# Optimization experiments

Hardware: AMD Instinct MI355X
Metric: run time of the kernel (lower is better)

## Reference

```python
import jax, jax.numpy as jnp
import numpy as np


def _rope_tables(seq_len, d_k, dtype):
    # Faithful to SimpleRotary intent: only d_k//4 frequencies exist; the
    # remaining d_k//4 of the half-width table is identity (cos=1, sin=0),
    # i.e. zero angular frequency (modded-nanogpt style partial rotary).
    half = d_k // 2
    quarter = d_k // 4
    freqs = (1.0 / 10000.0) ** np.linspace(0.0, 1.0, quarter, dtype=np.float32)
    ang = np.concatenate([freqs, np.zeros(half - quarter, dtype=np.float32)])
    theta = np.arange(seq_len, dtype=np.float32)[:, None] * ang[None, :]  # [S, d_k//2]
    return jnp.asarray(np.cos(theta), dtype), jnp.asarray(np.sin(theta), dtype)


def _apply_rope(x, cos, sin):
    # x: [B, H, S, d_k]; cos/sin: [S, d_k//2]
    x1, x2 = jnp.split(x, 2, axis=-1)
    c = cos[None, None]  # [1,1,S,d_k//2]
    s = sin[None, None]
    return jnp.concatenate([x1 * c - x2 * s, x1 * s + x2 * c], axis=-1)


def setup_inputs() -> dict:
    key = jax.random.key(0)
    k1, k2, k3 = jax.random.split(key, 3)
    B, S, D = 2, 2048, 1024
    x = jax.random.normal(k1, (B, S, D), dtype=jnp.float32)
    Wqkv = jax.random.normal(k2, (3 * D, D), dtype=jnp.float32) * 0.02
    Wo = jax.random.normal(k3, (D, D), dtype=jnp.float32) * 0.02
    return {"x": x, "Wqkv": Wqkv, "Wo": Wo, "n_heads": 16}


def reference(x, Wqkv, Wo, n_heads):
    B, S, D = x.shape
    d_k = D // n_heads
    qkv = jnp.einsum('bsd,ed->bse', x, Wqkv)  # [B,S,3D]
    qkv = qkv.reshape(B, S, 3, n_heads, d_k).transpose(2, 0, 3, 1, 4)  # [3,B,H,S,d_k]
    q, k, v = qkv[0], qkv[1], qkv[2]
    cos, sin = _rope_tables(S, d_k, x.dtype)
    q = _apply_rope(q, cos, sin)
    k = _apply_rope(k, cos, sin)
    scale = 1.0 / float(np.sqrt(d_k))
    scores = jnp.einsum('bhqd,bhkd->bhqk', q, k) * scale  # [B,H,S,S]
    causal = jnp.tril(jnp.ones((S, S), dtype=bool))
    scores = jnp.where(causal[None, None], scores, jnp.finfo(scores.dtype).min)
    probs = jax.nn.softmax(scores, axis=-1)
    out = jnp.einsum('bhqk,bhkd->bhqd', probs, v)  # [B,H,S,d_k]
    out = out.transpose(0, 2, 1, 3).reshape(B, S, D)
    return jnp.einsum('bsd,ed->bse', out, Wo)
```

## Files before the change

### kernel.cpp

```cpp
#include <hip/hip_runtime.h>
#include <hip/hip_bf16.h>


typedef __bf16 bf16x8 __attribute__((ext_vector_type(8)));
typedef float f32x4 __attribute__((ext_vector_type(4)));

#define LOG2E 1.4426950408889634f

__device__ __forceinline__ ushort f2bf(float f) {
  __hip_bfloat16 h = __float2bfloat16(f);
  return __builtin_bit_cast(ushort, h);
}

__device__ __forceinline__ uint pack2(float a, float b) {
  return (uint)f2bf(a) | ((uint)f2bf(b) << 16);
}

__device__ __forceinline__ uint pack2t(float a, float b) {
  return __builtin_amdgcn_perm(__builtin_bit_cast(uint, b),
                               __builtin_bit_cast(uint, a), 0x07060302u);
}

__device__ __forceinline__ float fexp2(float x) {
#if __has_builtin(__builtin_amdgcn_exp2f)
  return __builtin_amdgcn_exp2f(x);
#else
  float r;
  asm volatile("v_exp_f32 %0, %1\n\ts_nop 0" : "=v"(r) : "v"(x));
  return r;
#endif
}

#define CBAR() __asm__ __volatile__("" ::: "memory")

__device__ __forceinline__ void conv_frag_one(const float* __restrict__ src,
                                              ushort* __restrict__ dst, int b,
                                              int t) {
  int r16 = b >> 3, kc = b & 7;
  int c = t >> 6, lane = t & 63, quad = lane >> 4, rr = lane & 15;
  const float* s =
      src + ((long)(r16 * 16 + rr)) * 1024 + kc * 128 + c * 32 + quad * 8;
  float4 a = *(const float4*)s;
  float4 bb = *(const float4*)(s + 4);
  uint4 pk = {pack2(a.x, a.y), pack2(a.z, a.w), pack2(bb.x, bb.y),
              pack2(bb.z, bb.w)};
  *(uint4*)&dst[((long)(r16 * 32 + kc * 4 + c)) * 512 + lane * 8] = pk;
}

__global__ __launch_bounds__(256) void conv_frag3(
    const float* __restrict__ s0, ushort* __restrict__ d0, int nb0,
    const float* __restrict__ s1, ushort* __restrict__ d1, int nb1,
    const float* __restrict__ s2, ushort* __restrict__ d2) {
  int b = blockIdx.x;
  if (b < nb0) {
    conv_frag_one(s0, d0, b, threadIdx.x);
  } else if (b < nb0 + nb1) {
    conv_frag_one(s1, d1, b - nb0, threadIdx.x);
  } else {
    conv_frag_one(s2, d2, b - nb0 - nb1, threadIdx.x);
  }
}

__global__ __launch_bounds__(256) void gemm_bt(
    const ushort* __restrict__ A, const ushort* __restrict__ B,
    ushort* __restrict__ qb, ushort* __restrict__ kb, ushort* __restrict__ vb) {
  __shared__ __align__(16) ushort SMEM[17408];
  const int tid = threadIdx.x;
  const int w = tid >> 6, lane = tid & 63, quad = lane >> 4, lc = lane & 15;
  const int bid = blockIdx.x;
  const int bm = bid / 24, bn = bid % 24;
  const int wm = (w & 1) * 64, wn = (w >> 1) * 64;

  f32x4 acc[4][4] = {};

  const ushort* Ap = A + (long)(bm * 8 + (w & 1) * 4) * 16384 + lane * 8;
  const ushort* Bp = B + (long)(bn * 8 + (w >> 1) * 4) * 16384 + lane * 8;

#define GLD(AF, BF, K32)                                                       \
  {                                                                            \
    for (int t = 0; t < 4; ++t)                                                \
      AF[t] = *(const bf16x8*)&Ap[(long)t * 16384 + (K32) * 512];              \
    for (int t = 0; t < 4; ++t)                                                \
      BF[t] = *(const bf16x8*)&Bp[(long)t * 16384 + (K32) * 512];              \
  }
#define MM(AF, BF)                                                             \
  for (int rt = 0; rt < 4; ++rt)                                               \
    for (int ct = 0; ct < 4; ++ct)                                             \
      acc[rt][ct] = __builtin_amdgcn_mfma_f32_16x16x32_bf16(                   \
          AF[rt], BF[ct], acc[rt][ct], 0, 0, 0);

  bf16x8 a0[4], b0[4], a1[4], b1[4];
  GLD(a0, b0, 0);
  for (int k = 0; k < 32; k += 2) {
    GLD(a1, b1, k + 1);
    MM(a0, b0);
    int kn = (k + 2 < 32) ? k + 2 : 31;
    GLD(a0, b0, kn);
    MM(a1, b1);
  }
#undef GLD
#undef MM

  {
    const int e0 = bn * 128;
    const int g = e0 >> 10;
    const int h0 = (e0 & 1023) >> 6;
    ushort* Ct = SMEM;
    __syncthreads();

    if (g == 2) {
      for (int rt = 0; rt < 4; ++rt)
        for (int ct = 0; ct < 4; ++ct) {
          int col = wn + ct * 16 + lc;
          int r0 = wm + rt * 16 + quad * 4;
          uint2 pk = {pack2(acc[rt][ct][0], acc[rt][ct][1]),
                      pack2(acc[rt][ct][2], acc[rt][ct][3])};
          *(uint2*)&Ct[col * 136 + r0] = pk;
        }
    } else {
      const float qs = (g == 0) ? 0.125f * LOG2E : 1.0f;
      const float ang = powf(1e-4f, (float)lc * (1.0f / 15.0f));
      for (int rt = 0; rt < 4; ++rt)
        for (int r2 = 0; r2 < 4; ++r2) {
          int row = wm + rt * 16 + quad * 4 + r2;
          int srow = (bm * 128 + row) & 2047;
          float theta = (float)srow * ang;
          float sn, c;
          sincosf(theta, &sn, &c);
          float x1 = acc[rt][0][r2], x2 = acc[rt][2][r2];
          acc[rt][0][r2] = x1 * c - x2 * sn;
          acc[rt][2][r2] = x1 * sn + x2 * c;
          for (int ct = 0; ct < 4; ++ct)
            Ct[row * 136 + wn + ct * 16 + lc] = f2bf(acc[rt][ct][r2] * qs);
        }
    }
    __syncthreads();

    if (g == 0) {
      for (int i = 0; i < 8; ++i) {
        int u = i * 256 + tid;
        int row = u >> 4, c8 = u & 15;
        int m = bm * 128 + row;
        int srow = m & 2047, b = m >> 11;
        uint4 vv = *(const uint4*)&Ct[row * 136 + c8 * 8];
        *(uint4*)&qb[(((long)(b * 16 + h0 + (c8 >> 3))) * 2048 + srow) * 64 +
                     (c8 & 7) * 8] = vv;
      }
    } else if (g == 1) {
      for (int i = 0; i < 8; ++i) {
        int u = i * 256 + tid;
        int head = u >> 10, off = u & 1023;
        int jrel = off >> 9, kc = (off >> 8) & 1, t = (off >> 6) & 3;
        int quadK = (off >> 4) & 3, lcA = off & 15;
        int srl = jrel * 64 + t * 16 + lcA;
        uint4 vv = *(const uint4*)&Ct[srl * 136 + head * 64 + kc * 32 + quadK * 8];
        int m = bm * 128 + srl;
        int srow = m & 2047, b = m >> 11;
        int bh = b * 16 + h0 + head;
        int chunk = (srow >> 6) * 8 + kc * 4 + t;
        *(uint4*)&kb[(long)bh * 131072 + chunk * 512 + (quadK * 16 + lcA) * 8] = vv;
      }
    } else {
      for (int i = 0; i < 8; ++i) {
        int u = i * 256 + tid;
        int head = u >> 10, off = u & 1023;
        int jrel = off >> 9, kcV = (off >> 8) & 1, mt = (off >> 6) & 3;
        int quadV = (off >> 4) & 3, lcA = off & 15;
        int srl = jrel * 64 + kcV * 32 + quadV * 8;
        int d = mt * 16 + lcA;
        uint4 vv = *(const uint4*)&Ct[(head * 64 + d) * 136 + srl];
        int m = bm * 128 + srl;
        int srow = m & 2047, b = m >> 11;
        int bh = b * 16 + h0 + head;
        int chunk = (srow >> 6) * 8 + kcV * 4 + mt;
        *(uint4*)&vb[(long)bh * 131072 + chunk * 512 + (quadV * 16 + lcA) * 8] = vv;
      }
    }
  }
}

__global__ __launch_bounds__(64) void gemm_proj(
    const ushort* __restrict__ A, const ushort* __restrict__ B,
    float* __restrict__ Cout) {
  __shared__ __align__(16) float T[64 * 68];
  const int lane = threadIdx.x, quad = lane >> 4, lc = lane & 15;
  const int bid = blockIdx.x;
  const int r = bid >> 3;
  const int bm = (bid & 7) * 8 + (r >> 4);
  const int bn = r & 15;

  f32x4 acc[4][4] = {};

  const ushort* Ap = A + (long)(bm * 4) * 16384 + lane * 8;
  const ushort* Bp = B + (long)(bn * 4) * 16384 + lane * 8;

#define GLD(AF, BF, K32)                                                       \
  {                                                                            \
    for (int t = 0; t < 4; ++t)                                                \
      AF[t] = *(const bf16x8*)&Ap[(long)t * 16384 + (K32) * 512];              \
    for (int t = 0; t < 4; ++t)                                                \
      BF[t] = *(const bf16x8*)&Bp[(long)t * 16384 + (K32) * 512];              \
  }
#define MM(AF, BF)                                                             \
  for (int rt = 0; rt < 4; ++rt)                                               \
    for (int ct = 0; ct < 4; ++ct)                                             \
      acc[rt][ct] = __builtin_amdgcn_mfma_f32_16x16x32_bf16(                   \
          AF[rt], BF[ct], acc[rt][ct], 0, 0, 0);

  bf16x8 a0[4], b0[4], a1[4], b1[4];
  GLD(a0, b0, 0);
  for (int k = 0; k < 32; k += 2) {
    GLD(a1, b1, k + 1);
    MM(a0, b0);
    int kn = (k + 2 < 32) ? k + 2 : 31;
    GLD(a0, b0, kn);
    MM(a1, b1);
  }
#undef GLD
#undef MM

  for (int rt = 0; rt < 4; ++rt)
    for (int ct = 0; ct < 4; ++ct)
      for (int r2 = 0; r2 < 4; ++r2)
        T[(rt * 16 + quad * 4 + r2) * 68 + ct * 16 + lc] = acc[rt][ct][r2];
  CBAR();
  for (int p = 0; p < 16; ++p) {
    int row = p * 4 + quad;
    float4 v = *(const float4*)&T[row * 68 + lc * 4];
    *(float4*)&Cout[(long)(bm * 64 + row) * 1024 + bn * 64 + lc * 4] = v;
  }
}

__global__ __launch_bounds__(64) void attn_kernel(
    const ushort* __restrict__ qb, const ushort* __restrict__ kb,
    const ushort* __restrict__ vt, ushort* __restrict__ out) {
  __shared__ __align__(16) ushort Psw2[2][32 * 64];
  const int lane = threadIdx.x;
  const int quad = lane >> 4, lc = lane & 15, l7 = lc & 7;
  const int bid = blockIdx.x;
  const int s = 63 - (bid >> 5);
  const int bh = bid & 31;
  const int bidx = bh >> 4, h = bh & 15;
  const int qtbase = s * 32;

  bf16x8 qf[2][2];
  for (int kc = 0; kc < 2; ++kc)
    for (int q2 = 0; q2 < 2; ++q2)
      qf[kc][q2] = *(const bf16x8*)&qb[((long)bh * 2048 + qtbase + q2 * 16 + lc) * 64 +
                                       kc * 32 + quad * 8];

  f32x4 oacc[4][2] = {};
  float l_lane[2] = {0.0f, 0.0f};

  const ushort* K = kb + (long)bh * 131072;
  const ushort* Vt = vt + (long)bh * 131072;
  const int jmax = s >> 1;
  const int rowoff = (s & 1) * 32;
  const int lane8 = lane * 8;

#define LOADTILE(KF, VF, JT)                                                   \
  {                                                                            \
    const ushort* Kp_ = K + (JT) * 4096 + lane8;                               \
    const ushort* Vp_ = Vt + (JT) * 4096 + lane8;                              \
    for (int kc = 0; kc < 2; ++kc)                                             \
      for (int t = 0; t < 4; ++t) {                                            \
        KF[kc][t] = *(const bf16x8*)&Kp_[(kc * 4 + t) * 512];                  \
        VF[kc][t] = *(const bf16x8*)&Vp_[(kc * 4 + t) * 512];                  \
      }                                                                        \
  }

#define COMPUTE(KF, VF, J, PAR)                                                \
  {                                                                            \
    f32x4 sacc[4][2] = {};                                                     \
    __builtin_amdgcn_s_setprio(1);                                             \
    for (int kc = 0; kc < 2; ++kc)                                             \
      for (int kt = 0; kt < 4; ++kt)                                           \
        for (int q2 = 0; q2 < 2; ++q2)                                         \
          sacc[kt][q2] = __builtin_amdgcn_mfma_f32_16x16x32_bf16(              \
              KF[kc][kt], qf[kc][q2], sacc[kt][q2], 0, 0, 0);                  \
    __builtin_amdgcn_s_setprio(0);                                             \
    if ((J) == jmax) {                                \
      for (int kt = 0; kt < 4; ++kt)                                           \
        for (int q2 = 0; q2 < 2; ++q2) {                                       \
          int rowrel = rowoff + q2 * 16 + lc;                                  \
          for (int r = 0; r < 4; ++r)                                          \
            if (kt * 16 + quad * 4 + r > rowrel) sacc[kt][q2][r] = -1.0e30f;   \
        }                                                                      \
    }                                                                          \
    ushort* Psw = Psw2[PAR];                                                   \
    for (int q2 = 0; q2 < 2; ++q2) {                                           \
      float p[4][4];                                                           \
      float rs = 0.0f;                                                         \
      for (int kt = 0; kt < 4; ++kt)                                           \
        for (int r = 0; r < 4; ++r) {                                          \
          p[kt][r] = fexp2(sacc[kt][q2][r]);                                   \
          rs += p[kt][r];                                                      \
        }                                                                      \
      l_lane[q2] += rs;                                                        \
      for (int kt = 0; kt < 4; ++kt) {                                         \
        uint2 pk = {pack2t(p[kt][0], p[kt][1]), pack2t(p[kt][2], p[kt][3])};   \
        *(uint2*)&Psw[(q2 * 16 + lc) * 64 +                                    \
                      (((kt * 2 + (quad >> 1)) ^ l7) << 3) +                   \
                      ((quad & 1) << 2)] = pk;                                 \
      }                                                                        \
    }                                                                          \
    CBAR();       \
    __builtin_amdgcn_s_setprio(1);                                             \
    for (int kc = 0; kc < 2; ++kc) {                                           \
      bf16x8 pf[2];                                                            \
      for (int q2 = 0; q2 < 2; ++q2)                                           \
        pf[q2] = *(const bf16x8*)&Psw[(q2 * 16 + lc) * 64 +                    \
                                      (((kc * 4 + quad) ^ l7) << 3)];          \
      for (int mt = 0; mt < 4; ++mt)                                           \
        for (int q2 = 0; q2 < 2; ++q2)                                         \
          oacc[mt][q2] = __builtin_amdgcn_mfma_f32_16x16x32_bf16(              \
              VF[kc][mt], pf[q2], oacc[mt][q2], 0, 0, 0);                      \
    }                                                                          \
    __builtin_amdgcn_s_setprio(0);                                             \
  }

  bf16x8 kA[2][4], vA[2][4], kB[2][4], vB[2][4];
  LOADTILE(kA, vA, 0);
  int j = 0;
  while (true) {
    int jn = (j < jmax) ? j + 1 : j;
    LOADTILE(kB, vB, jn);
    COMPUTE(kA, vA, j, 0);
    if (j >= jmax) break;
    ++j;
    int jn2 = (j < jmax) ? j + 1 : j;
    LOADTILE(kA, vA, jn2);
    COMPUTE(kB, vB, j, 1);
    if (j >= jmax) break;
    ++j;
  }
#undef LOADTILE
#undef COMPUTE

  float l_[2];
  for (int q2 = 0; q2 < 2; ++q2) {
    float rs = l_lane[q2];
    rs += __shfl_xor(rs, 16, 64);
    rs += __shfl_xor(rs, 32, 64);
    l_[q2] = rs;
  }
  ushort* Psw = Psw2[0];
  CBAR();
  for (int q2 = 0; q2 < 2; ++q2) {
    float linv = 1.0f / l_[q2];
    for (int mt = 0; mt < 4; ++mt) {
      uint2 pk = {pack2(oacc[mt][q2][0] * linv, oacc[mt][q2][1] * linv),
                  pack2(oacc[mt][q2][2] * linv, oacc[mt][q2][3] * linv)};
      *(uint2*)&Psw[(q2 * 16 + lc) * 64 + (((mt * 2 + (quad >> 1)) ^ l7) << 3) +
                    ((quad & 1) << 2)] = pk;
    }
  }
  CBAR();
  {
    int r2 = lane >> 1;
    long m = (long)bidx * 2048 + qtbase + r2;
    int m4 = (int)(m >> 4), rr = (int)(m & 15);
    for (int c = 0; c < 4; ++c) {
      int c8 = (lane & 1) * 4 + c;
      uint4 vv = *(const uint4*)&Psw[r2 * 64 + ((c8 ^ (r2 & 7)) << 3)];
      *(uint4*)&out[((long)m4 * 32 + h * 2 + (c8 >> 2)) * 512 +
                    ((c8 & 3) * 16 + rr) * 8] = vv;
    }
  }
}

extern "C" void kernel_launch(void* const* d_in, const int* in_sizes, int n_in,
                              void* d_out, int out_size, void* d_ws, size_t ws_size,
                              hipStream_t stream) {
  const float* x = nullptr;
  const float* Wqkv = nullptr;
  const float* Wo = nullptr;
  for (int i = 0; i < n_in; ++i) {
    if (in_sizes[i] == 4194304) x = (const float*)d_in[i];
    else if (in_sizes[i] == 3145728) Wqkv = (const float*)d_in[i];
    else if (in_sizes[i] == 1048576) Wo = (const float*)d_in[i];
  }
  float* out = (float*)d_out;

  ushort* qbuf = (ushort*)d_ws;
  ushort* kbuf = qbuf + 4194304;
  ushort* vbuf = kbuf + 4194304;
  ushort* scr4 = vbuf + 4194304;
  ushort* wqkvh = scr4;
  ushort* ao   = scr4;
  ushort* xh   = (ushort*)d_out;
  ushort* woh  = xh + 4194304;

  conv_frag3<<<4096, 256, 0, stream>>>(x, xh, 2048, Wqkv, wqkvh, 1536, Wo, woh);
  gemm_bt<<<768, 256, 0, stream>>>(xh, wqkvh, qbuf, kbuf, vbuf);
  attn_kernel<<<2048, 64, 0, stream>>>(qbuf, kbuf, vbuf, ao);
  gemm_proj<<<1024, 64, 0, stream>>>(ao, woh, out);
}
```

Baseline: 189.1 us.

## Split attention KV loop across two waves with LDS reduction

The attention block grows from one wave to two. Each wave handles alternating KV tiles (even and odd) for the same 32 query rows, and the partial outputs and row sums are combined through shared memory before normalisation and the store. This is meant to shorten the serial KV loop per block on long causal rows and add more waves for latency hiding. In exchange it adds a cross-wave reduction, extra LDS, and __syncthreads. The first blocks (s=0,1) leave wave 1 idle. Since there is no max subtraction, the partial sums can be added directly.

```diff
diff --git a/kernel.cpp b/kernel.cpp
--- a/kernel.cpp
+++ b/kernel.cpp
@@ -231,32 +231,36 @@
   }
 }
 
-__global__ __launch_bounds__(64) void attn_kernel(
+__global__ __launch_bounds__(128) void attn_kernel(
     const ushort* __restrict__ qb, const ushort* __restrict__ kb,
     const ushort* __restrict__ vt, ushort* __restrict__ out) {
-  __shared__ __align__(16) ushort Psw2[2][32 * 64];
-  const int lane = threadIdx.x;
+  __shared__ __align__(16) ushort PswAll[2][2][32 * 64];
+  __shared__ float lbuf[128];
+  const int tid = threadIdx.x;
+  const int w = tid >> 6;
+  const int lane = tid & 63;
   const int quad = lane >> 4, lc = lane & 15, l7 = lc & 7;
   const int bid = blockIdx.x;
   const int s = 63 - (bid >> 5);
   const int bh = bid & 31;
   const int bidx = bh >> 4, h = bh & 15;
   const int qtbase = s * 32;
-
-  bf16x8 qf[2][2];
-  for (int kc = 0; kc < 2; ++kc)
-    for (int q2 = 0; q2 < 2; ++q2)
-      qf[kc][q2] = *(const bf16x8*)&qb[((long)bh * 2048 + qtbase + q2 * 16 + lc) * 64 +
-                                       kc * 32 + quad * 8];
-
-  f32x4 oacc[4][2] = {};
-  float l_lane[2] = {0.0f, 0.0f};
-
-  const ushort* K = kb + (long)bh * 131072;
-  const ushort* Vt = vt + (long)bh * 131072;
   const int jmax = s >> 1;
   const int rowoff = (s & 1) * 32;
   const int lane8 = lane * 8;
+
+  f32x4 oacc[4][2] = {};
+  float l_lane[2] = {0.0f, 0.0f};
+
+  const ushort* K = kb + (long)bh * 131072;
+  const ushort* Vt = vt + (long)bh * 131072;
+
+  if (w <= jmax) {
+    bf16x8 qf[2][2];
+    for (int kc = 0; kc < 2; ++kc)
+      for (int q2 = 0; q2 < 2; ++q2)
+        qf[kc][q2] = *(const bf16x8*)&qb[((long)bh * 2048 + qtbase + q2 * 16 + lc) * 64 +
+                                         kc * 32 + quad * 8];
 
 #define LOADTILE(KF, VF, JT)                                                   \
   {                                                                            \
@@ -279,7 +283,7 @@
           sacc[kt][q2] = __builtin_amdgcn_mfma_f32_16x16x32_bf16(              \
               KF[kc][kt], qf[kc][q2], sacc[kt][q2], 0, 0, 0);                  \
     __builtin_amdgcn_s_setprio(0);                                             \
-    if ((J) == jmax) {                                \
+    if ((J) == jmax) {              \
       for (int kt = 0; kt < 4; ++kt)                                           \
         for (int q2 = 0; q2 < 2; ++q2) {                                       \
           int rowrel = rowoff + q2 * 16 + lc;                                  \
@@ -287,7 +291,7 @@
             if (kt * 16 + quad * 4 + r > rowrel) sacc[kt][q2][r] = -1.0e30f;   \
         }                                                                      \
     }                                                                          \
-    ushort* Psw = Psw2[PAR];                                                   \
+    ushort* Psw = &PswAll[w][PAR][0];                                          \
     for (int q2 = 0; q2 < 2; ++q2) {                                           \
       float p[4][4];                                                           \
       float rs = 0.0f;                                                         \
@@ -304,7 +308,7 @@
                       ((quad & 1) << 2)] = pk;                                 \
       }                                                                        \
     }                                                                          \
-    CBAR();       \
+    CBAR();             \
     __builtin_amdgcn_s_setprio(1);                                             \
     for (int kc = 0; kc < 2; ++kc) {                                           \
       bf16x8 pf[2];                                                            \
@@ -319,23 +323,24 @@
     __builtin_amdgcn_s_setprio(0);                                             \
   }
 
-  bf16x8 kA[2][4], vA[2][4], kB[2][4], vB[2][4];
-  LOADTILE(kA, vA, 0);
-  int j = 0;
-  while (true) {
-    int jn = (j < jmax) ? j + 1 : j;
-    LOADTILE(kB, vB, jn);
-    COMPUTE(kA, vA, j, 0);
-    if (j >= jmax) break;
-    ++j;
-    int jn2 = (j < jmax) ? j + 1 : j;
-    LOADTILE(kA, vA, jn2);
-    COMPUTE(kB, vB, j, 1);
-    if (j >= jmax) break;
-    ++j;
-  }
+    bf16x8 kA[2][4], vA[2][4], kB[2][4], vB[2][4];
+    int j = w;
+    LOADTILE(kA, vA, j);
+    while (true) {
+      int jn = (j + 2 <= jmax) ? j + 2 : j;
+      LOADTILE(kB, vB, jn);
+      COMPUTE(kA, vA, j, 0);
+      if (j + 2 > jmax) break;
+      j += 2;
+      int jn2 = (j + 2 <= jmax) ? j + 2 : j;
+      LOADTILE(kA, vA, jn2);
+      COMPUTE(kB, vB, j, 1);
+      if (j + 2 > jmax) break;
+      j += 2;
+    }
 #undef LOADTILE
 #undef COMPUTE
+  }
 
   float l_[2];
   for (int q2 = 0; q2 < 2; ++q2) {
@@ -344,24 +349,44 @@
     rs += __shfl_xor(rs, 32, 64);
     l_[q2] = rs;
   }
-  ushort* Psw = Psw2[0];
-  CBAR();
-  for (int q2 = 0; q2 < 2; ++q2) {
-    float linv = 1.0f / l_[q2];
-    for (int mt = 0; mt < 4; ++mt) {
-      uint2 pk = {pack2(oacc[mt][q2][0] * linv, oacc[mt][q2][1] * linv),
-                  pack2(oacc[mt][q2][2] * linv, oacc[mt][q2][3] * linv)};
-      *(uint2*)&Psw[(q2 * 16 + lc) * 64 + (((mt * 2 + (quad >> 1)) ^ l7) << 3) +
-                    ((quad & 1) << 2)] = pk;
+
+  if (w == 1) {
+    float* Obuf = (float*)&PswAll[1][0][0];
+    for (int mt = 0; mt < 4; ++mt)
+      for (int q2 = 0; q2 < 2; ++q2)
+        *(f32x4*)&Obuf[(mt * 2 + q2) * 256 + lane * 4] = oacc[mt][q2];
+    lbuf[lane] = l_[0];
+    lbuf[64 + lane] = l_[1];
+  }
+  __syncthreads();
+
+  if (w == 0) {
+    const float* Obuf = (const float*)&PswAll[1][0][0];
+    for (int mt = 0; mt < 4; ++mt)
+      for (int q2 = 0; q2 < 2; ++q2)
+        oacc[mt][q2] += *(const f32x4*)&Obuf[(mt * 2 + q2) * 256 + lane * 4];
+    l_[0] += lbuf[lane];
+    l_[1] += lbuf[64 + lane];
+    ushort* Psw = &PswAll[0][0][0];
+    for (int q2 = 0; q2 < 2; ++q2) {
+      float linv = 1.0f / l_[q2];
+      for (int mt = 0; mt < 4; ++mt) {
+        uint2 pk = {pack2(oacc[mt][q2][0] * linv, oacc[mt][q2][1] * linv),
+                    pack2(oacc[mt][q2][2] * linv, oacc[mt][q2][3] * linv)};
+        *(uint2*)&Psw[(q2 * 16 + lc) * 64 + (((mt * 2 + (quad >> 1)) ^ l7) << 3) +
+                      ((quad & 1) << 2)] = pk;
+      }
     }
   }
-  CBAR();
+  __syncthreads();
+
   {
-    int r2 = lane >> 1;
+    const ushort* Psw = &PswAll[0][0][0];
+    int r2 = tid >> 2;
     long m = (long)bidx * 2048 + qtbase + r2;
     int m4 = (int)(m >> 4), rr = (int)(m & 15);
-    for (int c = 0; c < 4; ++c) {
-      int c8 = (lane & 1) * 4 + c;
+    for (int c = 0; c < 2; ++c) {
+      int c8 = (tid & 3) * 2 + c;
       uint4 vv = *(const uint4*)&Psw[r2 * 64 + ((c8 ^ (r2 & 7)) << 3)];
       *(uint4*)&out[((long)m4 * 32 + h * 2 + (c8 >> 2)) * 512 +
                     ((c8 & 3) * 16 + rr) * 8] = vv;
@@ -393,6 +418,6 @@
 
   conv_frag3<<<4096, 256, 0, stream>>>(x, xh, 2048, Wqkv, wqkvh, 1536, Wo, woh);
   gemm_bt<<<768, 256, 0, stream>>>(xh, wqkvh, qbuf, kbuf, vbuf);
-  attn_kernel<<<2048, 64, 0, stream>>>(qbuf, kbuf, vbuf, ao);
+  attn_kernel<<<2048, 128, 0, stream>>>(qbuf, kbuf, vbuf, ao);
   gemm_proj<<<1024, 64, 0, stream>>>(ao, woh, out);
 }
```

Result: slower. 198.1 us (+4.8%).
